# Kernel tuning notes

Hardware: AMD Instinct MI355X
Metric: run time of the kernel (lower is better)

## Reference

```python
import jax, jax.numpy as jnp
import numpy as np

N_NODES = 20000
N_EDGES = 320000
N_FEATS = 256
DIM_H = 64
HEADS = 8
N_CLASSES = 16
NEG_SLOPE = 0.2  # PyG GATv2Conv default negative_slope


def _glorot(key, shape):
    fan_in, fan_out = shape[0], shape[-1]
    lim = jnp.sqrt(6.0 / (fan_in + fan_out))
    return jax.random.uniform(key, shape, jnp.float32, -lim, lim)


def setup_inputs() -> dict:
    key = jax.random.key(0)
    ks = jax.random.split(key, 12)
    x = jax.random.normal(ks[0], (N_NODES, N_FEATS), jnp.float32)
    edge_index = jax.random.randint(ks[1], (2, N_EDGES), 0, N_NODES, jnp.int64)
    # layer 1: in=256 -> heads=8, out=64 (concat -> 512)
    W_l1 = _glorot(ks[2], (N_FEATS, HEADS * DIM_H))
    b_l1 = jnp.zeros((HEADS * DIM_H,), jnp.float32)
    W_r1 = _glorot(ks[3], (N_FEATS, HEADS * DIM_H))
    b_r1 = jnp.zeros((HEADS * DIM_H,), jnp.float32)
    att1 = _glorot(ks[4], (HEADS, DIM_H))
    bias1 = jnp.zeros((HEADS * DIM_H,), jnp.float32)
    # layer 2: in=512 -> heads=1, out=16
    W_l2 = _glorot(ks[5], (HEADS * DIM_H, N_CLASSES))
    b_l2 = jnp.zeros((N_CLASSES,), jnp.float32)
    W_r2 = _glorot(ks[6], (HEADS * DIM_H, N_CLASSES))
    b_r2 = jnp.zeros((N_CLASSES,), jnp.float32)
    att2 = _glorot(ks[7], (1, N_CLASSES))
    bias2 = jnp.zeros((N_CLASSES,), jnp.float32)
    return dict(x=x, edge_index=edge_index,
                W_l1=W_l1, b_l1=b_l1, W_r1=W_r1, b_r1=b_r1, att1=att1, bias1=bias1,
                W_l2=W_l2, b_l2=b_l2, W_r2=W_r2, b_r2=b_r2, att2=att2, bias2=bias2)


def gatv2_conv(x, src, dst, W_l, b_l, W_r, b_r, att, bias, n_nodes):
    """GATv2Conv (PyG defaults: share_weights=False, concat=True, no dropout in eval).
    src/dst already include self-loops. att: [H, D]."""
    H, D = att.shape
    x_l = (x @ W_l + b_l).reshape(n_nodes, H, D)  # source transform
    x_r = (x @ W_r + b_r).reshape(n_nodes, H, D)  # target transform
    # per-edge message: [E, H, D]
    m = jax.nn.leaky_relu(x_l[src] + x_r[dst], NEG_SLOPE)
    e = jnp.einsum('ehd,hd->eh', m, att)  # [E, H] attention logits
    # segment softmax over incoming edges of each dst node
    e_max = jax.ops.segment_max(e, dst, num_segments=n_nodes)  # [N, H]
    p = jnp.exp(e - e_max[dst])
    denom = jax.ops.segment_sum(p, dst, num_segments=n_nodes)  # [N, H]
    alpha = p / denom[dst]  # [E, H]
    out = jax.ops.segment_sum(alpha[:, :, None] * x_l[src], dst, num_segments=n_nodes)
    return out.reshape(n_nodes, H * D) + bias


def reference(x, edge_index, W_l1, b_l1, W_r1, b_r1, att1, bias1,
              W_l2, b_l2, W_r2, b_r2, att2, bias2):
    n = x.shape[0]
    loop = jnp.arange(n, dtype=edge_index.dtype)  # add_self_loops=True
    src = jnp.concatenate([edge_index[0], loop])
    dst = jnp.concatenate([edge_index[1], loop])
    h = gatv2_conv(x, src, dst, W_l1, b_l1, W_r1, b_r1, att1, bias1, n)
    h = jax.nn.relu(h)
    out = gatv2_conv(h, src, dst, W_l2, b_l2, W_r2, b_r2, att2, bias2, n)
    return out
```

## Files before the change

### kernel.cpp

```cpp
#include <hip/hip_runtime.h>
#include <hip/hip_bf16.h>
#include <stdint.h>

#define N_NODES 20000
#define MPAD    20096
#define N_EDG   320000
#define ET      (N_EDG + N_NODES)
#define NFE     256
#define HD      512
#define NH      8
#define DH      64
#define NC      16

typedef __attribute__((ext_vector_type(8))) short short8;
typedef __attribute__((ext_vector_type(8))) _Float16 half8;
typedef __attribute__((ext_vector_type(4))) float f32x4;

#define AS1 __attribute__((address_space(1)))
#define AS3 __attribute__((address_space(3)))

__device__ __forceinline__ unsigned short f2bf(float f) {
    unsigned u = __float_as_uint(f);
    return (unsigned short)((u + 0x7FFFu + ((u >> 16) & 1u)) >> 16);
}
__device__ __forceinline__ float bf2f(unsigned short s) {
    return __uint_as_float(((unsigned)s) << 16);
}

__global__ void count_deg(const int* __restrict__ ei, int* __restrict__ deg) {
    int e = blockIdx.x * 256 + threadIdx.x;
    if (e >= ET) return;
    int dst = (e < N_EDG) ? ei[N_EDG + e] : (e - N_EDG);
    atomicAdd(&deg[dst], 1);
}

__global__ __launch_bounds__(1024) void scan_offsets(const int* __restrict__ deg,
                                                     int* __restrict__ offs,
                                                     int* __restrict__ cur) {
    __shared__ int wsum[16];
    __shared__ int carry_s;
    int t = threadIdx.x;
    int wid = t >> 6, lane = t & 63;
    if (t == 0) { carry_s = 0; offs[0] = 0; }
    __syncthreads();
    for (int base = 0; base < N_NODES; base += 1024) {
        int i = base + t;
        int v = (i < N_NODES) ? deg[i] : 0;
        int sv = v;
        #pragma unroll
        for (int off = 1; off < 64; off <<= 1) {
            int n = __shfl_up(sv, off);
            if (lane >= off) sv += n;
        }
        if (lane == 63) wsum[wid] = sv;
        __syncthreads();
        int wpre = 0;
        #pragma unroll
        for (int w = 0; w < 16; ++w) wpre += (w < wid) ? wsum[w] : 0;
        int incl = sv + wpre + carry_s;
        if (i < N_NODES) {
            offs[i + 1] = incl;
            cur[i] = incl - v;
        }
        __syncthreads();
        if (t == 1023) carry_s = incl;
        __syncthreads();
    }
}

__global__ void fill_csr(const int* __restrict__ ei, int* __restrict__ cur,
                         int* __restrict__ esrc) {
    int e = blockIdx.x * 256 + threadIdx.x;
    if (e >= ET) return;
    int src, dst;
    if (e < N_EDG) { src = ei[e]; dst = ei[N_EDG + e]; }
    else { src = e - N_EDG; dst = src; }
    int pos = atomicAdd(&cur[dst], 1);
    esrc[pos] = src;
}

__global__ __launch_bounds__(256) void split_x(const float* __restrict__ x,
        unsigned short* __restrict__ xh, unsigned short* __restrict__ xl) {
    int i = (blockIdx.x * 256 + threadIdx.x) * 4;
    if (i >= N_NODES * NFE) return;
    float4 v = *reinterpret_cast<const float4*>(x + i);
    ushort4 h, l;
    h.x = f2bf(v.x); l.x = f2bf(v.x - bf2f(h.x));
    h.y = f2bf(v.y); l.y = f2bf(v.y - bf2f(h.y));
    h.z = f2bf(v.z); l.z = f2bf(v.z - bf2f(h.z));
    h.w = f2bf(v.w); l.w = f2bf(v.w - bf2f(h.w));
    *reinterpret_cast<ushort4*>(xh + i) = h;
    *reinterpret_cast<ushort4*>(xl + i) = l;
}

__global__ __launch_bounds__(256) void split_w(const float* __restrict__ Wl,
        const float* __restrict__ Wr, unsigned short* __restrict__ Wth,
        unsigned short* __restrict__ Wtl) {
    const float* W = blockIdx.y ? Wr : Wl;
    unsigned short* oh = Wth + (size_t)blockIdx.y * (HD * NFE);
    unsigned short* ol = Wtl + (size_t)blockIdx.y * (HD * NFE);
    int i = blockIdx.x * 256 + threadIdx.x;
    if (i >= NFE * HD) return;
    int k = i >> 9, n = i & 511;
    float v = W[i];
    unsigned short h = f2bf(v), l = f2bf(v - bf2f(h));
    oh[n * NFE + k] = h;
    ol[n * NFE + k] = l;
}

#define ROWP 157
#define G1_NWG (8 * ROWP * 2)
__global__ __launch_bounds__(256) void gemm1m(
        const unsigned short* __restrict__ xh, const unsigned short* __restrict__ xl,
        const unsigned short* __restrict__ Wth, const unsigned short* __restrict__ Wtl,
        const float* __restrict__ bl, const float* __restrict__ br,
        _Float16* __restrict__ outl, _Float16* __restrict__ outr) {
    __shared__ __align__(16) short Ah[2][128 * 32], Al[2][128 * 32];
    __shared__ __align__(16) short Bh[2][64 * 32],  Bls[2][64 * 32];

    int flat = blockIdx.x;
    int wgid = (flat & 7) * (G1_NWG / 8) + (flat >> 3);
    int z = wgid / (8 * ROWP);
    int rem = wgid - z * (8 * ROWP);
    int rowp = rem >> 3, colb = rem & 7;
    int row0 = rowp * 128, col0 = colb * 64;

    const unsigned short* Wh  = Wth + (size_t)z * (HD * NFE);
    const unsigned short* Wl_ = Wtl + (size_t)z * (HD * NFE);
    const float* bias = z ? br : bl;
    _Float16* out = z ? outr : outl;

    int tid = threadIdx.x;
    int w = tid >> 6, lane = tid & 63;
    int wr0 = (w >> 1) * 64, wn0 = (w & 1) * 32;
    int r16 = lane & 15, kb_l = lane >> 4;
    int rsub = lane >> 2, kch = lane & 3;

    f32x4 acc[4][2] = {};

    auto stage = [&](int buf, int k0) {
        #pragma unroll
        for (int i = 0; i < 2; ++i) {
            int inst = 2 * w + i;
            int rl = inst * 16 + rsub;
            size_t goff = (size_t)(row0 + rl) * NFE + k0 + kch * 8;
            __builtin_amdgcn_global_load_lds((const AS1 void*)(xh + goff),
                                             (AS3 void*)(&Ah[buf][inst * 512]), 16, 0, 0);
            __builtin_amdgcn_global_load_lds((const AS1 void*)(xl + goff),
                                             (AS3 void*)(&Al[buf][inst * 512]), 16, 0, 0);
        }
        int cl = w * 16 + rsub;
        size_t boff = (size_t)(col0 + cl) * NFE + k0 + kch * 8;
        __builtin_amdgcn_global_load_lds((const AS1 void*)(Wh + boff),
                                         (AS3 void*)(&Bh[buf][w * 512]), 16, 0, 0);
        __builtin_amdgcn_global_load_lds((const AS1 void*)(Wl_ + boff),
                                         (AS3 void*)(&Bls[buf][w * 512]), 16, 0, 0);
    };

    stage(0, 0);
    __syncthreads();

    for (int t = 0; t < 8; ++t) {
        int buf = t & 1;
        if (t < 7) stage(buf ^ 1, (t + 1) * 32);

        short8 ah[4], alv[4], bhv[2], blv[2];
        #pragma unroll
        for (int mi = 0; mi < 4; ++mi) {
            int idx = (wr0 + mi * 16 + r16) * 32 + kb_l * 8;
            ah[mi]  = *reinterpret_cast<const short8*>(&Ah[buf][idx]);
            alv[mi] = *reinterpret_cast<const short8*>(&Al[buf][idx]);
        }
        #pragma unroll
        for (int ni = 0; ni < 2; ++ni) {
            int idx = (wn0 + ni * 16 + r16) * 32 + kb_l * 8;
            bhv[ni] = *reinterpret_cast<const short8*>(&Bh[buf][idx]);
            blv[ni] = *reinterpret_cast<const short8*>(&Bls[buf][idx]);
        }
        #pragma unroll
        for (int mi = 0; mi < 4; ++mi)
            #pragma unroll
            for (int ni = 0; ni < 2; ++ni) {
                acc[mi][ni] = __builtin_amdgcn_mfma_f32_16x16x32_bf16(ah[mi],  bhv[ni], acc[mi][ni], 0, 0, 0);
                acc[mi][ni] = __builtin_amdgcn_mfma_f32_16x16x32_bf16(ah[mi],  blv[ni], acc[mi][ni], 0, 0, 0);
                acc[mi][ni] = __builtin_amdgcn_mfma_f32_16x16x32_bf16(alv[mi], bhv[ni], acc[mi][ni], 0, 0, 0);
            }
        __syncthreads();
    }

    int orow_base = row0 + wr0 + kb_l * 4;
    int ocol_base = col0 + wn0 + r16;
    #pragma unroll
    for (int mi = 0; mi < 4; ++mi)
        #pragma unroll
        for (int ni = 0; ni < 2; ++ni) {
            int col = ocol_base + ni * 16;
            float bv = bias[col];
            #pragma unroll
            for (int r = 0; r < 4; ++r) {
                int row = orow_base + mi * 16 + r;
                if (row < N_NODES)
                    out[(size_t)row * HD + col] = (_Float16)(acc[mi][ni][r] + bv);
            }
        }
}

__global__ __launch_bounds__(256) void fused1(const int* __restrict__ offs,
        const int* __restrict__ esrc,
        const _Float16* __restrict__ xl1, const _Float16* __restrict__ xr1,
        const float* __restrict__ att1, const float* __restrict__ bias1,
        float* __restrict__ hout) {
    int wid = (blockIdx.x * 256 + threadIdx.x) >> 6;
    int lane = threadIdx.x & 63;
    if (wid >= N_NODES) return;
    int beg = offs[wid], end = offs[wid + 1];

    float att[8], xr[8];
    *reinterpret_cast<float4*>(&att[0]) = *reinterpret_cast<const float4*>(att1 + lane * 8);
    *reinterpret_cast<float4*>(&att[4]) = *reinterpret_cast<const float4*>(att1 + lane * 8 + 4);
    {
        half8 hv = *reinterpret_cast<const half8*>(xr1 + (size_t)wid * HD + lane * 8);
        #pragma unroll
        for (int q = 0; q < 8; ++q) xr[q] = (float)hv[q];
    }

    float m = -3.4e38f, s = 0.f;
    float acc[8] = {};

    half8 xsp;
    xsp = *reinterpret_cast<const half8*>(xl1 + (size_t)esrc[beg] * HD + lane * 8);

    for (int j = beg; j < end; ++j) {
        half8 curh = xsp;
        if (j + 1 < end)
            xsp = *reinterpret_cast<const half8*>(xl1 + (size_t)esrc[j + 1] * HD + lane * 8);
        float cx[8];
        #pragma unroll
        for (int q = 0; q < 8; ++q) cx[q] = (float)curh[q];

        float v = 0.f;
        #pragma unroll
        for (int q = 0; q < 8; ++q) {
            float t = cx[q] + xr[q];
            t = t > 0.f ? t : 0.2f * t;
            v = fmaf(t, att[q], v);
        }
        v += __shfl_xor(v, 1);
        v += __shfl_xor(v, 2);
        v += __shfl_xor(v, 4);
        float nm = fmaxf(m, v);
        float sc = __expf(m - nm);
        float p  = __expf(v - nm);
        s = s * sc + p;
        #pragma unroll
        for (int q = 0; q < 8; ++q) acc[q] = fmaf(acc[q], sc, p * cx[q]);
        m = nm;
    }

    float inv = 1.0f / s;
    float o[8];
    #pragma unroll
    for (int q = 0; q < 8; ++q) {
        float bi = bias1[lane * 8 + q];
        o[q] = fmaxf(fmaf(acc[q], inv, bi), 0.f);
    }
    float* op = hout + (size_t)wid * HD + lane * 8;
    *reinterpret_cast<float4*>(op)     = *reinterpret_cast<float4*>(&o[0]);
    *reinterpret_cast<float4*>(op + 4) = *reinterpret_cast<float4*>(&o[4]);
}

__global__ __launch_bounds__(256) void gemm2(const float* __restrict__ h,
        const float* __restrict__ Wl2, const float* __restrict__ bl2,
        const float* __restrict__ Wr2, const float* __restrict__ br2,
        float* __restrict__ xl2, float* __restrict__ xr2) {
    int tx = threadIdx.x % 32;
    int ty = threadIdx.x / 32;
    int row = blockIdx.x * 8 + ty;
    if (row >= N_NODES) return;
    const float* W = (tx < 16) ? Wl2 : Wr2;
    int c = tx & 15;
    const float4* hr4 = reinterpret_cast<const float4*>(h + (size_t)row * HD);
    float acc = 0.f;
    #pragma unroll 4
    for (int k4 = 0; k4 < HD / 4; ++k4) {
        float4 v = hr4[k4];
        int k = k4 * 4;
        acc = fmaf(v.x, W[(k + 0) * NC + c], acc);
        acc = fmaf(v.y, W[(k + 1) * NC + c], acc);
        acc = fmaf(v.z, W[(k + 2) * NC + c], acc);
        acc = fmaf(v.w, W[(k + 3) * NC + c], acc);
    }
    if (tx < 16) xl2[(size_t)row * NC + c] = acc + bl2[c];
    else         xr2[(size_t)row * NC + c] = acc + br2[c];
}

__global__ __launch_bounds__(256) void fused2(const int* __restrict__ offs,
        const int* __restrict__ esrc,
        const float* __restrict__ xl2, const float* __restrict__ xr2,
        const float* __restrict__ att2, const float* __restrict__ bias2,
        float* __restrict__ out) {
    int wid = (blockIdx.x * 256 + threadIdx.x) >> 6;
    int lane = threadIdx.x & 63;
    if (wid >= N_NODES) return;
    int g = lane >> 4, d = lane & 15;
    int beg = offs[wid], end = offs[wid + 1];

    float xr = xr2[(size_t)wid * NC + d];
    float at = att2[d];
    float m = -3.4e38f, s = 0.f, acc = 0.f;

    for (int j = beg + g; j < end; j += 4) {
        int src = esrc[j];
        float xs = xl2[(size_t)src * NC + d];
        float t = xs + xr;
        t = t > 0.f ? t : 0.2f * t;
        float v = t * at;
        v += __shfl_xor(v, 1);
        v += __shfl_xor(v, 2);
        v += __shfl_xor(v, 4);
        v += __shfl_xor(v, 8);
        float nm = fmaxf(m, v);
        float sc = __expf(m - nm), p = __expf(v - nm);
        s = s * sc + p;
        acc = fmaf(acc, sc, p * xs);
        m = nm;
    }
    #pragma unroll
    for (int off = 16; off < 64; off <<= 1) {
        float om = __shfl_xor(m, off);
        float os = __shfl_xor(s, off);
        float oa = __shfl_xor(acc, off);
        float nm = fmaxf(m, om);
        float c1 = __expf(m - nm), c2 = __expf(om - nm);
        s = s * c1 + os * c2;
        acc = acc * c1 + oa * c2;
        m = nm;
    }
    if (lane < 16) out[(size_t)wid * NC + d] = acc / s + bias2[d];
}

extern "C" void kernel_launch(void* const* d_in, const int* in_sizes, int n_in,
                              void* d_out, int out_size, void* d_ws, size_t ws_size,
                              hipStream_t stream) {
    const float* x     = (const float*)d_in[0];
    const int*   ei    = (const int*)d_in[1];
    const float* W_l1  = (const float*)d_in[2];
    const float* b_l1  = (const float*)d_in[3];
    const float* W_r1  = (const float*)d_in[4];
    const float* b_r1  = (const float*)d_in[5];
    const float* att1  = (const float*)d_in[6];
    const float* bias1 = (const float*)d_in[7];
    const float* W_l2  = (const float*)d_in[8];
    const float* b_l2  = (const float*)d_in[9];
    const float* W_r2  = (const float*)d_in[10];
    const float* b_r2  = (const float*)d_in[11];
    const float* att2  = (const float*)d_in[12];
    const float* bias2 = (const float*)d_in[13];
    float* out = (float*)d_out;

    char* ws = (char*)d_ws;
    _Float16* xl1 = (_Float16*)ws; ws += (size_t)N_NODES * HD * sizeof(_Float16);
    _Float16* xr1 = (_Float16*)ws; ws += (size_t)N_NODES * HD * sizeof(_Float16);
    float* hbuf = (float*)ws; ws += (size_t)N_NODES * HD * sizeof(float);
    float* xl2  = (float*)ws; ws += (size_t)N_NODES * NC * sizeof(float);
    float* xr2  = (float*)ws; ws += (size_t)N_NODES * NC * sizeof(float);
    int* deg    = (int*)ws; ws += (size_t)N_NODES * sizeof(int);
    int* offs   = (int*)ws; ws += (size_t)(N_NODES + 1) * sizeof(int);
    int* cursor = (int*)ws; ws += (size_t)N_NODES * sizeof(int);
    int* esrc   = (int*)ws; ws += (size_t)ET * sizeof(int);
    unsigned short* xh  = (unsigned short*)ws; ws += (size_t)MPAD * NFE * sizeof(short);
    unsigned short* xlo = (unsigned short*)ws; ws += (size_t)MPAD * NFE * sizeof(short);
    unsigned short* Wth = (unsigned short*)ws; ws += (size_t)2 * HD * NFE * sizeof(short);
    unsigned short* Wtl = (unsigned short*)ws; ws += (size_t)2 * HD * NFE * sizeof(short);

    hipMemsetAsync(deg, 0, N_NODES * sizeof(int), stream);
    count_deg<<<(ET + 255) / 256, 256, 0, stream>>>(ei, deg);
    scan_offsets<<<1, 1024, 0, stream>>>(deg, offs, cursor);
    fill_csr<<<(ET + 255) / 256, 256, 0, stream>>>(ei, cursor, esrc);

    split_x<<<(N_NODES * NFE / 4 + 255) / 256, 256, 0, stream>>>(x, xh, xlo);
    split_w<<<dim3((NFE * HD + 255) / 256, 2), 256, 0, stream>>>(W_l1, W_r1, Wth, Wtl);

    gemm1m<<<G1_NWG, 256, 0, stream>>>(xh, xlo, Wth, Wtl, b_l1, b_r1, xl1, xr1);
    fused1<<<(N_NODES + 3) / 4, 256, 0, stream>>>(offs, esrc, xl1, xr1, att1, bias1, hbuf);

    gemm2<<<(N_NODES + 7) / 8, 256, 0, stream>>>(hbuf, W_l2, b_l2, W_r2, b_r2, xl2, xr2);
    fused2<<<(N_NODES + 3) / 4, 256, 0, stream>>>(offs, esrc, xl2, xr2, att2, bias2, out);
}
```

Measured before the change: 366.2 us.

## Fuse layer-2 linear projections into layer-1 aggregation epilogue

The fused1 kernel now applies the layer-2 weight matrices directly to the per-node hidden vector it holds in registers. It reduces across the wave with butterfly shuffles and writes xl2/xr2, so the separate gemm2 kernel and the 20000x512 fp32 hidden buffer round trip go away. In exchange, each wave runs 8 full 64-lane shuffle reductions (each over four values) per node. Every lane also reads a slice of the 512x16 weight matrices, which adds ALU and shuffle work to the aggregation kernel.

```diff
diff --git a/kernel.cpp b/kernel.cpp
--- a/kernel.cpp
+++ b/kernel.cpp
@@ -209,7 +209,9 @@
         const int* __restrict__ esrc,
         const _Float16* __restrict__ xl1, const _Float16* __restrict__ xr1,
         const float* __restrict__ att1, const float* __restrict__ bias1,
-        float* __restrict__ hout) {
+        const float* __restrict__ Wl2, const float* __restrict__ bl2,
+        const float* __restrict__ Wr2, const float* __restrict__ br2,
+        float* __restrict__ xl2, float* __restrict__ xr2) {
     int wid = (blockIdx.x * 256 + threadIdx.x) >> 6;
     int lane = threadIdx.x & 63;
     if (wid >= N_NODES) return;
@@ -258,40 +260,44 @@
     }
 
     float inv = 1.0f / s;
-    float o[8];
+    float h[8];
     #pragma unroll
     for (int q = 0; q < 8; ++q) {
         float bi = bias1[lane * 8 + q];
-        o[q] = fmaxf(fmaf(acc[q], inv, bi), 0.f);
-    }
-    float* op = hout + (size_t)wid * HD + lane * 8;
-    *reinterpret_cast<float4*>(op)     = *reinterpret_cast<float4*>(&o[0]);
-    *reinterpret_cast<float4*>(op + 4) = *reinterpret_cast<float4*>(&o[4]);
-}
-
-__global__ __launch_bounds__(256) void gemm2(const float* __restrict__ h,
-        const float* __restrict__ Wl2, const float* __restrict__ bl2,
-        const float* __restrict__ Wr2, const float* __restrict__ br2,
-        float* __restrict__ xl2, float* __restrict__ xr2) {
-    int tx = threadIdx.x % 32;
-    int ty = threadIdx.x / 32;
-    int row = blockIdx.x * 8 + ty;
-    if (row >= N_NODES) return;
-    const float* W = (tx < 16) ? Wl2 : Wr2;
-    int c = tx & 15;
-    const float4* hr4 = reinterpret_cast<const float4*>(h + (size_t)row * HD);
-    float acc = 0.f;
-    #pragma unroll 4
-    for (int k4 = 0; k4 < HD / 4; ++k4) {
-        float4 v = hr4[k4];
-        int k = k4 * 4;
-        acc = fmaf(v.x, W[(k + 0) * NC + c], acc);
-        acc = fmaf(v.y, W[(k + 1) * NC + c], acc);
-        acc = fmaf(v.z, W[(k + 2) * NC + c], acc);
-        acc = fmaf(v.w, W[(k + 3) * NC + c], acc);
-    }
-    if (tx < 16) xl2[(size_t)row * NC + c] = acc + bl2[c];
-    else         xr2[(size_t)row * NC + c] = acc + br2[c];
+        h[q] = fmaxf(fmaf(acc[q], inv, bi), 0.f);
+    }
+
+    int rowb = lane * 8;
+    #pragma unroll
+    for (int mat = 0; mat < 2; ++mat) {
+        const float* W = mat ? Wr2 : Wl2;
+        const float* b2 = mat ? br2 : bl2;
+        float* o2 = mat ? xr2 : xl2;
+        #pragma unroll
+        for (int cb = 0; cb < 4; ++cb) {
+            float4 part = make_float4(0.f, 0.f, 0.f, 0.f);
+            #pragma unroll
+            for (int q = 0; q < 8; ++q) {
+                float4 wv = *reinterpret_cast<const float4*>(W + (size_t)(rowb + q) * NC + cb * 4);
+                part.x = fmaf(h[q], wv.x, part.x);
+                part.y = fmaf(h[q], wv.y, part.y);
+                part.z = fmaf(h[q], wv.z, part.z);
+                part.w = fmaf(h[q], wv.w, part.w);
+            }
+            #pragma unroll
+            for (int st = 1; st < 64; st <<= 1) {
+                part.x += __shfl_xor(part.x, st);
+                part.y += __shfl_xor(part.y, st);
+                part.z += __shfl_xor(part.z, st);
+                part.w += __shfl_xor(part.w, st);
+            }
+            if (lane == cb) {
+                float4 bv = *reinterpret_cast<const float4*>(b2 + cb * 4);
+                part.x += bv.x; part.y += bv.y; part.z += bv.z; part.w += bv.w;
+                *reinterpret_cast<float4*>(o2 + (size_t)wid * NC + cb * 4) = part;
+            }
+        }
+    }
 }
 
 __global__ __launch_bounds__(256) void fused2(const int* __restrict__ offs,
@@ -361,7 +367,6 @@
     char* ws = (char*)d_ws;
     _Float16* xl1 = (_Float16*)ws; ws += (size_t)N_NODES * HD * sizeof(_Float16);
     _Float16* xr1 = (_Float16*)ws; ws += (size_t)N_NODES * HD * sizeof(_Float16);
-    float* hbuf = (float*)ws; ws += (size_t)N_NODES * HD * sizeof(float);
     float* xl2  = (float*)ws; ws += (size_t)N_NODES * NC * sizeof(float);
     float* xr2  = (float*)ws; ws += (size_t)N_NODES * NC * sizeof(float);
     int* deg    = (int*)ws; ws += (size_t)N_NODES * sizeof(int);
@@ -382,8 +387,7 @@
     split_w<<<dim3((NFE * HD + 255) / 256, 2), 256, 0, stream>>>(W_l1, W_r1, Wth, Wtl);
 
     gemm1m<<<G1_NWG, 256, 0, stream>>>(xh, xlo, Wth, Wtl, b_l1, b_r1, xl1, xr1);
-    fused1<<<(N_NODES + 3) / 4, 256, 0, stream>>>(offs, esrc, xl1, xr1, att1, bias1, hbuf);
-
-    gemm2<<<(N_NODES + 7) / 8, 256, 0, stream>>>(hbuf, W_l2, b_l2, W_r2, b_r2, xl2, xr2);
+    fused1<<<(N_NODES + 3) / 4, 256, 0, stream>>>(offs, esrc, xl1, xr1, att1, bias1,
+                                                  W_l2, b_l2, W_r2, b_r2, xl2, xr2);
     fused2<<<(N_NODES + 3) / 4, 256, 0, stream>>>(offs, esrc, xl2, xr2, att2, bias2, out);
 }
```

Result: slower. 431.7 us (+17.9%).
